# Optimization experiments

Measured on AMD Instinct MI355X. Metric: run time of the kernel, lower is better.

The kernel has to match this reference:

```python
import jax, jax.numpy as jnp
import numpy as np

N_THETA = 180  # matches init kwarg n_theta


def setup_inputs() -> dict:
    key = jax.random.key(0)
    image = jax.random.normal(key, (2, 1, 256, 256), dtype=jnp.float32)
    return {"image": image}


def _radon_forward(image):
    # image: [B, 1, W, W]
    B, _, W, _ = image.shape
    # circle=False: pad to the diagonal so rotation never clips content
    diag = 2.0 ** 0.5 * W
    pad = int(np.ceil(diag - W))
    S = int(np.ceil(diag))                    # padded square size (363 for W=256)
    new_center = (W + pad) // 2
    pad_before = new_center - W // 2
    pad_after = pad - pad_before
    img = jnp.pad(image[:, 0], ((0, 0), (pad_before, pad_after), (pad_before, pad_after)))  # [B,S,S]

    thetas = jnp.deg2rad(jnp.linspace(0.0, 180.0, N_THETA))
    cos_a = jnp.cos(thetas)[:, None, None]    # [A,1,1]
    sin_a = jnp.sin(thetas)[:, None, None]

    # torch affine_grid(align_corners=True): base grid in [-1,1] inclusive
    base = jnp.linspace(-1.0, 1.0, S)
    y = base[:, None]                          # height index i
    x = base[None, :]                          # width index j
    # theta = [[c, s, 0], [-s, c, 0]] -> sample coords per angle, [A,S,S]
    gx = cos_a * x + sin_a * y
    gy = -sin_a * x + cos_a * y

    # grid_sample align_corners=True: pixel coord = (g+1)/2*(S-1)
    px = (gx + 1.0) * 0.5 * (S - 1)
    py = (gy + 1.0) * 0.5 * (S - 1)
    x0 = jnp.floor(px).astype(jnp.int32); x1 = x0 + 1
    y0 = jnp.floor(py).astype(jnp.int32); y1 = y0 + 1
    wx1 = px - x0; wx0 = 1.0 - wx1
    wy1 = py - y0; wy0 = 1.0 - wy1

    def fetch(yi, xi):
        # zeros padding: out-of-range taps contribute 0
        valid = ((yi >= 0) & (yi < S) & (xi >= 0) & (xi < S)).astype(img.dtype)
        yc = jnp.clip(yi, 0, S - 1)
        xc = jnp.clip(xi, 0, S - 1)
        return img[:, yc, xc] * valid[None]    # [B,A,S,S]

    sampled = (fetch(y0, x0) * (wy0 * wx0)[None]
               + fetch(y0, x1) * (wy0 * wx1)[None]
               + fetch(y1, x0) * (wy1 * wx0)[None]
               + fetch(y1, x1) * (wy1 * wx1)[None])   # [B,A,S,S]

    sino = sampled.sum(axis=2)                 # sum over height -> [B,A,S]
    # torch: stack along dim=2 then permute(0,1,3,2) -> [B,1,S,A]
    return jnp.transpose(sino, (0, 2, 1))[:, None]


def reference(image):
    return _radon_forward(image)
```

## Files before the change

kernel.cpp:

```cpp
#include <hip/hip_runtime.h>
#include <math.h>
#include <stdint.h>


#define SS 363
#define WW 256
#define NT 180
#define AP 9
#define QDIM (WW + 2 * AP)
#define QCNT (QDIM * QDIM)

typedef _Float16 h8 __attribute__((ext_vector_type(8)));
typedef __fp16  h2 __attribute__((ext_vector_type(2)));

#if defined(__has_builtin)
#if __has_builtin(__builtin_amdgcn_fdot2) && __has_builtin(__builtin_amdgcn_cvt_pkrtz)
#define USE_DOT2 1
#endif
#endif

__global__ __launch_bounds__(256) void radon_prep(const float* __restrict__ img,
                                                  h8* __restrict__ q) {
    const int idx = blockIdx.x * 256 + threadIdx.x;
    if (idx >= QCNT) return;
    const int iy = idx / QDIM;
    const int ix = idx - iy * QDIM;
    const int y0 = iy - AP, x0 = ix - AP;
    const bool xin0 = ((unsigned)x0 < (unsigned)WW);
    const bool xin1 = ((unsigned)(x0 + 1) < (unsigned)WW);
    const bool yin0 = ((unsigned)y0 < (unsigned)WW);
    const bool yin1 = ((unsigned)(y0 + 1) < (unsigned)WW);
    h8 o;
    #pragma unroll
    for (int b = 0; b < 2; ++b) {
        const float* __restrict__ im = img + b * WW * WW;
        float v00 = 0.f, v01 = 0.f, v10 = 0.f, v11 = 0.f;
        if (yin0) {
            const float* r0 = im + y0 * WW;
            if (xin0) v00 = r0[x0];
            if (xin1) v01 = r0[x0 + 1];
        }
        if (yin1) {
            const float* r1 = im + (y0 + 1) * WW;
            if (xin0) v10 = r1[x0];
            if (xin1) v11 = r1[x0 + 1];
        }
        o[4 * b + 0] = (_Float16)v00;
        o[4 * b + 1] = (_Float16)v01;
        o[4 * b + 2] = (_Float16)v10;
        o[4 * b + 3] = (_Float16)v11;
    }
    q[idx] = o;
}

__global__ __launch_bounds__(256) void radon_main(const h8* __restrict__ q,
                                                  float* __restrict__ out) {
    const int tid = threadIdx.x;
    const int w   = tid >> 6;
    const int l   = tid & 63;
    const int cl  = l & 7;
    const int rl  = l >> 3;
    const int tile = blockIdx.x * 4 + w;
    if (tile * 8 >= SS) return;
    const int t = blockIdx.y;
    const int c = tile * 8 + cl;

    float sv, cv;
    sincosf((float)t * 0.017551608191455498f, &sv, &cv);
    const float x   = fmaf((float)c, 0.0055248618784530386f, -1.0f);
    const float gx0 = fmaf(cv, x, -sv);
    const float gy0 = fmaf(-sv, x, -cv);
    const float px0 = fmaf(gx0, 181.0f, 128.0f);
    const float py0 = fmaf(gy0, 181.0f, 128.0f);

    float rlo = 0.0f, rhi = 362.0f;
    if (fabsf(sv) > 1e-8f) {
        const float ra = (-1.0f - px0) / sv, rb = (256.0f - px0) / sv;
        rlo = fmaxf(rlo, fminf(ra, rb)); rhi = fminf(rhi, fmaxf(ra, rb));
    } else if (px0 <= -1.0f || px0 >= 256.0f) rhi = -2.0f;
    if (fabsf(cv) > 1e-8f) {
        const float ra = (-1.0f - py0) / cv, rb = (256.0f - py0) / cv;
        rlo = fmaxf(rlo, fminf(ra, rb)); rhi = fminf(rhi, fmaxf(ra, rb));
    } else if (py0 <= -1.0f || py0 >= 256.0f) rhi = -2.0f;
    int Rlo = max(0, (int)floorf(rlo) - 1);
    int Rhi = min(SS - 1, (int)ceilf(rhi) + 1);
    #pragma unroll
    for (int o = 1; o <= 4; o <<= 1) {
        Rlo = min(Rlo, __shfl_xor(Rlo, o, 64));
        Rhi = max(Rhi, __shfl_xor(Rhi, o, 64));
    }

    const uint4* __restrict__ qb = (const uint4*)q;
    const int base_off = AP * QDIM + AP;
    float acc0 = 0.0f, acc1 = 0.0f;
    #pragma unroll 2
    for (int r = Rlo + rl; r <= Rhi; r += 8) {
        const float rf = (float)r;
        const float px = fmaf(rf, sv, px0);
        const float py = fmaf(rf, cv, py0);
        const float fx = floorf(px), fy = floorf(py);
        const float wx1 = px - fx, wy1 = py - fy;
        const float wx0 = 1.0f - wx1, wy0 = 1.0f - wy1;
        const int idx = (int)fmaf(fy, (float)QDIM, fx) + base_off;
        const uint4 u = qb[idx];
#ifdef USE_DOT2
        const h2 wlo = __builtin_amdgcn_cvt_pkrtz(wy0 * wx0, wy0 * wx1);
        const h2 whi = __builtin_amdgcn_cvt_pkrtz(wy1 * wx0, wy1 * wx1);
        acc0 = __builtin_amdgcn_fdot2(wlo, __builtin_bit_cast(h2, u.x), acc0, false);
        acc0 = __builtin_amdgcn_fdot2(whi, __builtin_bit_cast(h2, u.y), acc0, false);
        acc1 = __builtin_amdgcn_fdot2(wlo, __builtin_bit_cast(h2, u.z), acc1, false);
        acc1 = __builtin_amdgcn_fdot2(whi, __builtin_bit_cast(h2, u.w), acc1, false);
#else
        const h2 v01 = __builtin_bit_cast(h2, u.x);
        const h2 v23 = __builtin_bit_cast(h2, u.y);
        const h2 v45 = __builtin_bit_cast(h2, u.z);
        const h2 v67 = __builtin_bit_cast(h2, u.w);
        const float top0 = fmaf(wx0, (float)v01[0], wx1 * (float)v01[1]);
        const float bot0 = fmaf(wx0, (float)v23[0], wx1 * (float)v23[1]);
        acc0 = fmaf(wy0, top0, acc0);
        acc0 = fmaf(wy1, bot0, acc0);
        const float top1 = fmaf(wx0, (float)v45[0], wx1 * (float)v45[1]);
        const float bot1 = fmaf(wx0, (float)v67[0], wx1 * (float)v67[1]);
        acc1 = fmaf(wy0, top1, acc1);
        acc1 = fmaf(wy1, bot1, acc1);
#endif
    }
    acc0 += __shfl_xor(acc0, 8, 64);
    acc0 += __shfl_xor(acc0, 16, 64);
    acc0 += __shfl_xor(acc0, 32, 64);
    acc1 += __shfl_xor(acc1, 8, 64);
    acc1 += __shfl_xor(acc1, 16, 64);
    acc1 += __shfl_xor(acc1, 32, 64);
    if (l < 8) {
        const int cc = tile * 8 + l;
        if (cc < SS) {
            out[(0 * SS + cc) * NT + t] = acc0;
            out[(1 * SS + cc) * NT + t] = acc1;
        }
    }
}

__global__ __launch_bounds__(256) void radon_fwd_fb(const float* __restrict__ img,
                                                    float* __restrict__ out) {
    const int tid = threadIdx.x;
    const int w = tid >> 6, l = tid & 63, cl = l & 7, rl = l >> 3;
    const int c0 = blockIdx.x * 8, c = c0 + cl, t = blockIdx.y, b = blockIdx.z;
    float sv, cv;
    sincosf((float)t * 0.017551608191455498f, &sv, &cv);
    const float x   = fmaf((float)c, 0.0055248618784530386f, -1.0f);
    const float px0 = fmaf(fmaf(cv, x, -sv), 181.0f, 128.0f);
    const float py0 = fmaf(fmaf(-sv, x, -cv), 181.0f, 128.0f);
    float rlo = 0.0f, rhi = 362.0f;
    if (fabsf(sv) > 1e-8f) {
        const float ra = (-1.0f - px0) / sv, rb = (256.0f - px0) / sv;
        rlo = fmaxf(rlo, fminf(ra, rb)); rhi = fminf(rhi, fmaxf(ra, rb));
    } else if (px0 <= -1.0f || px0 >= 256.0f) rhi = -2.0f;
    if (fabsf(cv) > 1e-8f) {
        const float ra = (-1.0f - py0) / cv, rb = (256.0f - py0) / cv;
        rlo = fmaxf(rlo, fminf(ra, rb)); rhi = fminf(rhi, fmaxf(ra, rb));
    } else if (py0 <= -1.0f || py0 >= 256.0f) rhi = -2.0f;
    int Rlo = max(0, (int)floorf(rlo) - 1);
    int Rhi = min(SS - 1, (int)ceilf(rhi) + 1);
    #pragma unroll
    for (int o = 1; o <= 4; o <<= 1) {
        Rlo = min(Rlo, __shfl_xor(Rlo, o, 64));
        Rhi = max(Rhi, __shfl_xor(Rhi, o, 64));
    }
    const float* __restrict__ imgb = img + b * (WW * WW);
    float acc = 0.0f;
    for (int r = Rlo + 8 * w + rl; r <= Rhi; r += 32) {
        const float rf = (float)r;
        const float px = fmaf(rf, sv, px0), py = fmaf(rf, cv, py0);
        const float fx = floorf(px), fy = floorf(py);
        float wx1 = px - fx, wy1 = py - fy;
        float wx0 = 1.0f - wx1, wy0 = 1.0f - wy1;
        const int x0 = (int)fx, y0 = (int)fy, x1 = x0 + 1, y1 = y0 + 1;
        wx0 *= ((unsigned)x0 < (unsigned)WW) ? 1.0f : 0.0f;
        wx1 *= ((unsigned)x1 < (unsigned)WW) ? 1.0f : 0.0f;
        wy0 *= ((unsigned)y0 < (unsigned)WW) ? 1.0f : 0.0f;
        wy1 *= ((unsigned)y1 < (unsigned)WW) ? 1.0f : 0.0f;
        const int xc0 = min(max(x0, 0), WW - 1), xc1 = min(max(x1, 0), WW - 1);
        const int yc0 = min(max(y0, 0), WW - 1), yc1 = min(max(y1, 0), WW - 1);
        const float* r0p = imgb + yc0 * WW;
        const float* r1p = imgb + yc1 * WW;
        const float top = fmaf(wx0, r0p[xc0], wx1 * r0p[xc1]);
        const float bot = fmaf(wx0, r1p[xc0], wx1 * r1p[xc1]);
        acc = fmaf(wy0, top, acc);
        acc = fmaf(wy1, bot, acc);
    }
    acc += __shfl_xor(acc, 8, 64);
    acc += __shfl_xor(acc, 16, 64);
    acc += __shfl_xor(acc, 32, 64);
    __shared__ float part[4][8];
    if (l < 8) part[w][l] = acc;
    __syncthreads();
    if (tid < 8) {
        const int cc = c0 + tid;
        if (cc < SS)
            out[(b * SS + cc) * NT + t] =
                part[0][tid] + part[1][tid] + part[2][tid] + part[3][tid];
    }
}

extern "C" void kernel_launch(void* const* d_in, const int* in_sizes, int n_in,
                              void* d_out, int out_size, void* d_ws, size_t ws_size,
                              hipStream_t stream) {
    (void)in_sizes; (void)n_in; (void)out_size;
    const float* img = (const float*)d_in[0];
    float* out = (float*)d_out;
    const size_t need = (size_t)QCNT * sizeof(h8);
    if (ws_size >= need) {
        h8* q = (h8*)d_ws;
        hipLaunchKernelGGL(radon_prep, dim3((QCNT + 255) / 256), dim3(256), 0,
                           stream, img, q);
        const int ntile = (SS + 7) / 8;
        dim3 grid((ntile + 3) / 4, NT, 1);
        hipLaunchKernelGGL(radon_main, grid, dim3(256), 0, stream, q, out);
    } else {
        dim3 grid((SS + 7) / 8, NT, 2);
        hipLaunchKernelGGL(radon_fwd_fb, grid, dim3(256), 0, stream, img, out);
    }
}
```

Measured before the change: 72.06 us.

## Precompute per-angle trig and ray ranges in prep; split rows across waves

The prep kernel gains extra blocks that compute sin/cos per angle and the union of valid row ranges per 8-column tile, and store them in the workspace. The main kernel reads these values instead of recomputing them. It now gives each 256-thread block a single tile, with the four waves interleaving rows, and combines their partial sums through shared memory. This spreads each column's row loop over four times as many threads and drops the per-thread trig and range math. The cost is a barrier, a shared-memory reduction, four times as many blocks, and a larger workspace requirement.

```diff
diff --git a/kernel.cpp b/kernel.cpp
--- a/kernel.cpp
+++ b/kernel.cpp
@@ -9,6 +9,15 @@
 #define AP 9
 #define QDIM (WW + 2 * AP)
 #define QCNT (QDIM * QDIM)
+#define NTILE 46
+#define NRANGE (NT * NTILE)
+#define NBQ ((QCNT + 255) / 256)
+#define NBR ((NRANGE + 255) / 256)
+
+#define QOFF 0
+#define SCOFF (QCNT * 16)
+#define RGOFF (SCOFF + ((NT * 8 + 15) & ~15))
+#define WSNEED (RGOFF + NRANGE * 4)
 
 typedef _Float16 h8 __attribute__((ext_vector_type(8)));
 typedef __fp16  h2 __attribute__((ext_vector_type(2)));
@@ -20,81 +29,100 @@
 #endif
 
 __global__ __launch_bounds__(256) void radon_prep(const float* __restrict__ img,
-                                                  h8* __restrict__ q) {
-    const int idx = blockIdx.x * 256 + threadIdx.x;
-    if (idx >= QCNT) return;
-    const int iy = idx / QDIM;
-    const int ix = idx - iy * QDIM;
-    const int y0 = iy - AP, x0 = ix - AP;
-    const bool xin0 = ((unsigned)x0 < (unsigned)WW);
-    const bool xin1 = ((unsigned)(x0 + 1) < (unsigned)WW);
-    const bool yin0 = ((unsigned)y0 < (unsigned)WW);
-    const bool yin1 = ((unsigned)(y0 + 1) < (unsigned)WW);
-    h8 o;
-    #pragma unroll
-    for (int b = 0; b < 2; ++b) {
-        const float* __restrict__ im = img + b * WW * WW;
-        float v00 = 0.f, v01 = 0.f, v10 = 0.f, v11 = 0.f;
-        if (yin0) {
-            const float* r0 = im + y0 * WW;
-            if (xin0) v00 = r0[x0];
-            if (xin1) v01 = r0[x0 + 1];
+                                                  char* __restrict__ ws) {
+    h8* __restrict__ q = (h8*)(ws + QOFF);
+    if (blockIdx.x < NBQ) {
+        const int idx = blockIdx.x * 256 + threadIdx.x;
+        if (idx >= QCNT) return;
+        const int iy = idx / QDIM;
+        const int ix = idx - iy * QDIM;
+        const int y0 = iy - AP, x0 = ix - AP;
+        const bool xin0 = ((unsigned)x0 < (unsigned)WW);
+        const bool xin1 = ((unsigned)(x0 + 1) < (unsigned)WW);
+        const bool yin0 = ((unsigned)y0 < (unsigned)WW);
+        const bool yin1 = ((unsigned)(y0 + 1) < (unsigned)WW);
+        h8 o;
+        #pragma unroll
+        for (int b = 0; b < 2; ++b) {
+            const float* __restrict__ im = img + b * WW * WW;
+            float v00 = 0.f, v01 = 0.f, v10 = 0.f, v11 = 0.f;
+            if (yin0) {
+                const float* r0 = im + y0 * WW;
+                if (xin0) v00 = r0[x0];
+                if (xin1) v01 = r0[x0 + 1];
+            }
+            if (yin1) {
+                const float* r1 = im + (y0 + 1) * WW;
+                if (xin0) v10 = r1[x0];
+                if (xin1) v11 = r1[x0 + 1];
+            }
+            o[4 * b + 0] = (_Float16)v00;
+            o[4 * b + 1] = (_Float16)v01;
+            o[4 * b + 2] = (_Float16)v10;
+            o[4 * b + 3] = (_Float16)v11;
         }
-        if (yin1) {
-            const float* r1 = im + (y0 + 1) * WW;
-            if (xin0) v10 = r1[x0];
-            if (xin1) v11 = r1[x0 + 1];
+        q[idx] = o;
+    } else {
+        const int ridx = (blockIdx.x - NBQ) * 256 + threadIdx.x;
+        if (ridx >= NRANGE) return;
+        const int t    = ridx / NTILE;
+        const int tile = ridx - t * NTILE;
+        float sv, cv;
+        sincosf((float)t * 0.017551608191455498f, &sv, &cv);
+        if (tile == 0) ((float2*)(ws + SCOFF))[t] = make_float2(sv, cv);
+        int Ulo = SS;
+        int Uhi = -1;
+        #pragma unroll
+        for (int cl = 0; cl < 8; ++cl) {
+            const int c = tile * 8 + cl;
+            const float x   = fmaf((float)c, 0.0055248618784530386f, -1.0f);
+            const float px0 = fmaf(fmaf(cv, x, -sv), 181.0f, 128.0f);
+            const float py0 = fmaf(fmaf(-sv, x, -cv), 181.0f, 128.0f);
+            float rlo = 0.0f, rhi = 362.0f;
+            if (fabsf(sv) > 1e-8f) {
+                const float ra = (-1.0f - px0) / sv, rb = (256.0f - px0) / sv;
+                rlo = fmaxf(rlo, fminf(ra, rb)); rhi = fminf(rhi, fmaxf(ra, rb));
+            } else if (px0 <= -1.0f || px0 >= 256.0f) rhi = -2.0f;
+            if (fabsf(cv) > 1e-8f) {
+                const float ra = (-1.0f - py0) / cv, rb = (256.0f - py0) / cv;
+                rlo = fmaxf(rlo, fminf(ra, rb)); rhi = fminf(rhi, fmaxf(ra, rb));
+            } else if (py0 <= -1.0f || py0 >= 256.0f) rhi = -2.0f;
+            const int Rlo = min(max(0, (int)floorf(rlo) - 1), SS);
+            const int Rhi = max(min(SS - 1, (int)ceilf(rhi) + 1), -1);
+            Ulo = min(Ulo, Rlo);
+            Uhi = max(Uhi, Rhi);
         }
-        o[4 * b + 0] = (_Float16)v00;
-        o[4 * b + 1] = (_Float16)v01;
-        o[4 * b + 2] = (_Float16)v10;
-        o[4 * b + 3] = (_Float16)v11;
-    }
-    q[idx] = o;
-}
-
-__global__ __launch_bounds__(256) void radon_main(const h8* __restrict__ q,
+        ((int*)(ws + RGOFF))[ridx] =
+            ((int)(unsigned short)(short)Ulo) | ((int)(short)Uhi << 16);
+    }
+}
+
+__global__ __launch_bounds__(256) void radon_main(const char* __restrict__ ws,
                                                   float* __restrict__ out) {
     const int tid = threadIdx.x;
     const int w   = tid >> 6;
     const int l   = tid & 63;
     const int cl  = l & 7;
     const int rl  = l >> 3;
-    const int tile = blockIdx.x * 4 + w;
-    if (tile * 8 >= SS) return;
-    const int t = blockIdx.y;
+    const int tile = blockIdx.x;
+    const int t    = blockIdx.y;
+
+    const float2 sc = ((const float2*)(ws + SCOFF))[t];
+    const float sv = sc.x, cv = sc.y;
+    const int rr = ((const int*)(ws + RGOFF))[t * NTILE + tile];
+    const int Rlo = (int)(short)(rr & 0xffff);
+    const int Rhi = rr >> 16;
+
     const int c = tile * 8 + cl;
-
-    float sv, cv;
-    sincosf((float)t * 0.017551608191455498f, &sv, &cv);
     const float x   = fmaf((float)c, 0.0055248618784530386f, -1.0f);
-    const float gx0 = fmaf(cv, x, -sv);
-    const float gy0 = fmaf(-sv, x, -cv);
-    const float px0 = fmaf(gx0, 181.0f, 128.0f);
-    const float py0 = fmaf(gy0, 181.0f, 128.0f);
-
-    float rlo = 0.0f, rhi = 362.0f;
-    if (fabsf(sv) > 1e-8f) {
-        const float ra = (-1.0f - px0) / sv, rb = (256.0f - px0) / sv;
-        rlo = fmaxf(rlo, fminf(ra, rb)); rhi = fminf(rhi, fmaxf(ra, rb));
-    } else if (px0 <= -1.0f || px0 >= 256.0f) rhi = -2.0f;
-    if (fabsf(cv) > 1e-8f) {
-        const float ra = (-1.0f - py0) / cv, rb = (256.0f - py0) / cv;
-        rlo = fmaxf(rlo, fminf(ra, rb)); rhi = fminf(rhi, fmaxf(ra, rb));
-    } else if (py0 <= -1.0f || py0 >= 256.0f) rhi = -2.0f;
-    int Rlo = max(0, (int)floorf(rlo) - 1);
-    int Rhi = min(SS - 1, (int)ceilf(rhi) + 1);
-    #pragma unroll
-    for (int o = 1; o <= 4; o <<= 1) {
-        Rlo = min(Rlo, __shfl_xor(Rlo, o, 64));
-        Rhi = max(Rhi, __shfl_xor(Rhi, o, 64));
-    }
-
-    const uint4* __restrict__ qb = (const uint4*)q;
+    const float px0 = fmaf(fmaf(cv, x, -sv), 181.0f, 128.0f);
+    const float py0 = fmaf(fmaf(-sv, x, -cv), 181.0f, 128.0f);
+
+    const uint4* __restrict__ qb = (const uint4*)(ws + QOFF);
     const int base_off = AP * QDIM + AP;
     float acc0 = 0.0f, acc1 = 0.0f;
     #pragma unroll 2
-    for (int r = Rlo + rl; r <= Rhi; r += 8) {
+    for (int r = Rlo + rl + 8 * w; r <= Rhi; r += 32) {
         const float rf = (float)r;
         const float px = fmaf(rf, sv, px0);
         const float py = fmaf(rf, cv, py0);
@@ -131,11 +159,17 @@
     acc1 += __shfl_xor(acc1, 8, 64);
     acc1 += __shfl_xor(acc1, 16, 64);
     acc1 += __shfl_xor(acc1, 32, 64);
-    if (l < 8) {
-        const int cc = tile * 8 + l;
+
+    __shared__ float p0[4][8], p1[4][8];
+    if (l < 8) { p0[w][l] = acc0; p1[w][l] = acc1; }
+    __syncthreads();
+    if (tid < 8) {
+        const int cc = tile * 8 + tid;
         if (cc < SS) {
-            out[(0 * SS + cc) * NT + t] = acc0;
-            out[(1 * SS + cc) * NT + t] = acc1;
+            out[(0 * SS + cc) * NT + t] =
+                p0[0][tid] + p0[1][tid] + p0[2][tid] + p0[3][tid];
+            out[(1 * SS + cc) * NT + t] =
+                p1[0][tid] + p1[1][tid] + p1[2][tid] + p1[3][tid];
         }
     }
 }
@@ -208,14 +242,12 @@
     (void)in_sizes; (void)n_in; (void)out_size;
     const float* img = (const float*)d_in[0];
     float* out = (float*)d_out;
-    const size_t need = (size_t)QCNT * sizeof(h8);
-    if (ws_size >= need) {
-        h8* q = (h8*)d_ws;
-        hipLaunchKernelGGL(radon_prep, dim3((QCNT + 255) / 256), dim3(256), 0,
-                           stream, img, q);
-        const int ntile = (SS + 7) / 8;
-        dim3 grid((ntile + 3) / 4, NT, 1);
-        hipLaunchKernelGGL(radon_main, grid, dim3(256), 0, stream, q, out);
+    if (ws_size >= (size_t)WSNEED) {
+        char* ws = (char*)d_ws;
+        hipLaunchKernelGGL(radon_prep, dim3(NBQ + NBR), dim3(256), 0,
+                           stream, img, ws);
+        dim3 grid(NTILE, NT, 1);
+        hipLaunchKernelGGL(radon_main, grid, dim3(256), 0, stream, ws, out);
     } else {
         dim3 grid((SS + 7) / 8, NT, 2);
         hipLaunchKernelGGL(radon_fwd_fb, grid, dim3(256), 0, stream, img, out);
```

New measurement: 71.91 us, median of 2. About the same (-0.2%).
